# Kernel optimization log

Hardware: AMD Instinct MI355X
Metric: run time of the kernel (lower is better)

Reference implementation:

```python
import jax, jax.numpy as jnp
import numpy as np

B, T, C = 16, 2048, 68
HEAD = 64

def setup_inputs() -> dict:
    key = jax.random.key(0)
    k1, k2, k3, k4 = jax.random.split(key, 4)
    x = jax.random.normal(k1, (B, T, C), dtype=jnp.float32)
    # Linear(n_embd, head_size, bias=False): y = x @ W, W stored as [C, HEAD]
    Wk = jax.random.normal(k2, (C, HEAD), dtype=jnp.float32) / np.sqrt(C)
    Wq = jax.random.normal(k3, (C, HEAD), dtype=jnp.float32) / np.sqrt(C)
    Wv = jax.random.normal(k4, (C, HEAD), dtype=jnp.float32) / np.sqrt(C)
    return {"x": x, "Wk": Wk, "Wq": Wq, "Wv": Wv}

def reference(x, Wk, Wq, Wv):
    # single-head attention, no causal mask, dropout p=0.0 (identity)
    k = jnp.einsum('btc,ch->bth', x, Wk)   # [B,T,H]
    q = jnp.einsum('btc,ch->bth', x, Wq)   # [B,T,H]
    v = jnp.einsum('btc,ch->bth', x, Wv)   # [B,T,H]
    scale = 1.0 / jnp.sqrt(jnp.asarray(k.shape[-1], k.dtype))
    wei = jnp.einsum('bqh,bkh->bqk', q, k) * scale  # [B,T,T]
    wei = jax.nn.softmax(wei, axis=-1)
    out = jnp.einsum('bqk,bkh->bqh', wei, v)        # [B,T,H]
    return out
```

## Files before the change

### kernel.cpp

```cpp
#include <hip/hip_runtime.h>
#include <hip/hip_bf16.h>

#define BB 16
#define TT 2048
#define CC 68
#define HH 64

typedef short short8 __attribute__((ext_vector_type(8)));
typedef float floatx4 __attribute__((ext_vector_type(4)));

static __device__ __forceinline__ unsigned short f2bf(float f) {
    union { float f; unsigned u; } v; v.f = f;
    unsigned r = v.u + 0x7fffu + ((v.u >> 16) & 1u);
    return (unsigned short)(r >> 16);
}
static __device__ __forceinline__ unsigned pk2(float a, float b) {
    unsigned ua = __builtin_bit_cast(unsigned, a) + 0x8000u;
    unsigned ub = __builtin_bit_cast(unsigned, b) + 0x8000u;
    return (ua >> 16) | (ub & 0xffff0000u);
}
static __device__ __forceinline__ unsigned cvtpk(float a, float b) {
    unsigned r;
    asm("v_cvt_pk_bf16_f32 %0, %1, %2" : "=v"(r) : "v"(a), "v"(b));
    return r;
}

#define GLD16(gsrc, ldsbase)                                                        \
    __builtin_amdgcn_global_load_lds(                                               \
        (const __attribute__((address_space(1))) unsigned int*)(gsrc),              \
        (__attribute__((address_space(3))) unsigned int*)(ldsbase), 16, 0, 0)

#define WAITV4 asm volatile("s_waitcnt vmcnt(4)" ::: "memory")
#define WAITV0 asm volatile("s_waitcnt vmcnt(0)" ::: "memory")
#define BAR    asm volatile("s_barrier" ::: "memory")

__global__ __launch_bounds__(256) void prep_w(
        const float* __restrict__ Wk, const float* __restrict__ Wq,
        const float* __restrict__ Wv, unsigned short* __restrict__ Wt) {
    int idx = blockIdx.x * 256 + threadIdx.x;
    if (idx >= 192 * 96) return;
    int n = idx / 96, c = idx - n * 96;
    float v = 0.f;
    if (c < CC) {
        if (n < 64)       v = Wk[c * 64 + n];
        else if (n < 128) v = Wq[c * 64 + (n - 64)] * 0.18033688011112042f;
        else              v = Wv[c * 64 + (n - 128)];
    }
    Wt[idx] = f2bf(v);
}

__global__ __launch_bounds__(256) void qkv_kernel(
        const float* __restrict__ x, const unsigned short* __restrict__ Wt,
        unsigned short* __restrict__ Qb, unsigned short* __restrict__ Kb,
        unsigned short* __restrict__ Vt) {
    int tid = threadIdx.x;
    int wave = tid >> 6, lane = tid & 63, quad = lane >> 4, l15 = lane & 15;
    int id = blockIdx.x;
    int b = id & 15, rowblk = id >> 4;
    size_t row0 = (size_t)b * TT + rowblk * 64;
    int t0 = rowblk * 64;
    size_t myrow = row0 + wave * 16 + l15;
    const float* xr = x + myrow * CC;

    short8 a[3];
    union { short8 s8; unsigned u[4]; } t;
    #pragma unroll
    for (int cs = 0; cs < 2; ++cs) {
        float4 f0 = *(const float4*)(xr + cs * 32 + quad * 8);
        float4 f1 = *(const float4*)(xr + cs * 32 + quad * 8 + 4);
        t.u[0] = pk2(f0.x, f0.y); t.u[1] = pk2(f0.z, f0.w);
        t.u[2] = pk2(f1.x, f1.y); t.u[3] = pk2(f1.z, f1.w);
        a[cs] = t.s8;
    }
    {
        t.u[0] = 0; t.u[1] = 0; t.u[2] = 0; t.u[3] = 0;
        if (quad == 0) {
            float4 f = *(const float4*)(xr + 64);
            t.u[0] = pk2(f.x, f.y); t.u[1] = pk2(f.z, f.w);
        }
        a[2] = t.s8;
    }

    auto loadW = [&](short8 (&w)[3], int nt) {
        #pragma unroll
        for (int cs = 0; cs < 3; ++cs)
            w[cs] = *(const short8*)&Wt[(nt * 16 + l15) * 96 + cs * 32 + quad * 8];
    };

    short8 wf[3][3];
    loadW(wf[0], 0);
    loadW(wf[1], 1);
    #pragma unroll
    for (int nt = 0; nt < 12; ++nt) {
        if (nt + 2 < 12) loadW(wf[(nt + 2) % 3], nt + 2);
        floatx4 acc = (floatx4){0.f, 0.f, 0.f, 0.f};
        #pragma unroll
        for (int cs = 0; cs < 3; ++cs)
            acc = __builtin_amdgcn_mfma_f32_16x16x32_bf16(a[cs], wf[nt % 3][cs], acc, 0, 0, 0);

        if (nt < 8) {
            unsigned short* dst = (nt < 4) ? Kb : Qb;
            int h = (nt & 3) * 16 + l15;
            #pragma unroll
            for (int r = 0; r < 4; ++r)
                dst[(row0 + wave * 16 + quad * 4 + r) * 64 + h] = f2bf(acc[r]);
        } else {
            int h = (nt - 8) * 16 + l15;
            int tt = t0 + wave * 16 + quad * 4;
            uint2 v2; v2.x = pk2(acc[0], acc[1]); v2.y = pk2(acc[2], acc[3]);
            *(uint2*)&Vt[((size_t)(b * 64 + h)) * TT + tt] = v2;
        }
    }
}

__global__ __launch_bounds__(512, 2) void attn_kernel(
        const unsigned short* __restrict__ Qb,
        const unsigned short* __restrict__ Kb,
        const unsigned short* __restrict__ Vt,
        float* __restrict__ out) {
    __shared__ union {
        unsigned char stg[2][3][8192];
        float accL[128][66];
    } u;
    __shared__ float lL[2][128];

    int tid = threadIdx.x;
    int wave = tid >> 6, lane = tid & 63, quad = lane >> 4, l15 = lane & 15;
    int half = wave >> 2, qh = wave & 3;
    int id = blockIdx.x;
    int b = id & 15, qblk = id >> 4;
    int q0 = qblk * 128 + qh * 32;
    int kbase = half * 1024;

    short8 qf[2][2];
    #pragma unroll
    for (int qs = 0; qs < 2; ++qs)
        #pragma unroll
        for (int kh = 0; kh < 2; ++kh)
            qf[qs][kh] = *(const short8*)&Qb[((size_t)(b * TT + q0 + qs * 16 + l15)) * 64
                                             + kh * 32 + quad * 8];

    floatx4 acc[2][4];
    float lpart[2] = {0.f, 0.f};
    #pragma unroll
    for (int qs = 0; qs < 2; ++qs)
        #pragma unroll
        for (int hb = 0; hb < 4; ++hb) acc[qs][hb] = (floatx4){0.f, 0.f, 0.f, 0.f};

    auto stage = [&](int it, int p) {
        int kt = kbase + it * 32;
        if (qh == 0) {
            unsigned char* base = u.stg[half][p];
            #pragma unroll
            for (int i = 0; i < 4; ++i) {
                int ci = i * 64 + lane;
                int kv = ci >> 3, cp = ci & 7, c = cp ^ (kv & 7);
                GLD16(Kb + ((size_t)(b * TT + kt + kv) * 64 + c * 8), base + i * 1024);
            }
        } else if (qh == 1) {
            unsigned char* base = u.stg[half][p] + 4096;
            #pragma unroll
            for (int i = 0; i < 4; ++i) {
                int ci = i * 64 + lane;
                int h = ci >> 2, cp = ci & 3, c = cp ^ ((h >> 1) & 3);
                GLD16(Vt + ((size_t)(b * 64 + h) * TT + kt + c * 8), base + i * 1024);
            }
        }
    };

    auto compute = [&](int p) {
        const unsigned char* Kbuf = u.stg[half][p];
        const unsigned char* Vbuf = Kbuf + 4096;

        short8 kf[2][2], vf[4];
        #pragma unroll
        for (int ks = 0; ks < 2; ++ks)
            #pragma unroll
            for (int kh = 0; kh < 2; ++kh) {
                int cp = (kh * 4 + quad) ^ (l15 & 7);
                kf[ks][kh] = *(const short8*)(Kbuf + (ks * 16 + l15) * 128 + cp * 16);
            }
        #pragma unroll
        for (int hb = 0; hb < 4; ++hb) {
            int cp = quad ^ ((l15 >> 1) & 3);
            vf[hb] = *(const short8*)(Vbuf + (hb * 16 + l15) * 64 + cp * 16);
        }

        floatx4 s[2][2];
        #pragma unroll
        for (int qs = 0; qs < 2; ++qs)
            #pragma unroll
            for (int ks = 0; ks < 2; ++ks) {
                floatx4 z = (floatx4){0.f, 0.f, 0.f, 0.f};
                z = __builtin_amdgcn_mfma_f32_16x16x32_bf16(kf[ks][0], qf[qs][0], z, 0, 0, 0);
                z = __builtin_amdgcn_mfma_f32_16x16x32_bf16(kf[ks][1], qf[qs][1], z, 0, 0, 0);
                s[qs][ks] = z;
            }

        #pragma unroll
        for (int qs = 0; qs < 2; ++qs) {
            unsigned c00, c01, c10, c11;
            float lp = 0.f;
            {
                float e0 = __builtin_amdgcn_exp2f(s[qs][0][0]);
                float e1 = __builtin_amdgcn_exp2f(s[qs][0][1]);
                float e2 = __builtin_amdgcn_exp2f(s[qs][0][2]);
                float e3 = __builtin_amdgcn_exp2f(s[qs][0][3]);
                lp += (e0 + e1) + (e2 + e3);
                c00 = cvtpk(e0, e1); c01 = cvtpk(e2, e3);
            }
            {
                float e0 = __builtin_amdgcn_exp2f(s[qs][1][0]);
                float e1 = __builtin_amdgcn_exp2f(s[qs][1][1]);
                float e2 = __builtin_amdgcn_exp2f(s[qs][1][2]);
                float e3 = __builtin_amdgcn_exp2f(s[qs][1][3]);
                lp += (e0 + e1) + (e2 + e3);
                c10 = cvtpk(e0, e1); c11 = cvtpk(e2, e3);
            }
            lpart[qs] += lp;

            asm("v_permlane32_swap_b32 %0, %1" : "+v"(c00), "+v"(c10));
            asm("v_permlane16_swap_b32 %0, %1" : "+v"(c00), "+v"(c10));
            asm("v_permlane32_swap_b32 %0, %1" : "+v"(c01), "+v"(c11));
            asm("v_permlane16_swap_b32 %0, %1" : "+v"(c01), "+v"(c11));

            union { short8 s8; unsigned w[4]; } pu;
            pu.w[0] = c00; pu.w[1] = c01; pu.w[2] = c10; pu.w[3] = c11;
            #pragma unroll
            for (int hb = 0; hb < 4; ++hb)
                acc[qs][hb] = __builtin_amdgcn_mfma_f32_16x16x32_bf16(pu.s8, vf[hb], acc[qs][hb], 0, 0, 0);
        }
    };

    stage(0, 0);
    stage(1, 1);
    for (int it = 0; it < 32; ++it) {
        if (qh < 2) {
            if (it < 31) { WAITV4; } else { WAITV0; }
        }
        BAR;
        if (it + 2 < 32) stage(it + 2, (it + 2) % 3);
        compute(it % 3);
    }

    #pragma unroll
    for (int qs = 0; qs < 2; ++qs) {
        float v = lpart[qs];
        v += __shfl_xor(v, 16);
        v += __shfl_xor(v, 32);
        lpart[qs] = v;
    }
    if (quad == 0) {
        lL[half][qh * 32 + l15]      = lpart[0];
        lL[half][qh * 32 + 16 + l15] = lpart[1];
    }
    __syncthreads();

    if (half == 1) {
        #pragma unroll
        for (int qs = 0; qs < 2; ++qs)
            #pragma unroll
            for (int hb = 0; hb < 4; ++hb)
                #pragma unroll
                for (int r = 0; r < 4; ++r)
                    u.accL[qh * 32 + qs * 16 + quad * 4 + r][hb * 16 + l15] = acc[qs][hb][r];
    }
    __syncthreads();

    if (half == 0) {
        #pragma unroll
        for (int qs = 0; qs < 2; ++qs) {
            float rl[4];
            #pragma unroll
            for (int r = 0; r < 4; ++r) {
                int qw = qh * 32 + qs * 16 + quad * 4 + r;
                rl[r] = 1.0f / (lL[0][qw] + lL[1][qw]);
            }
            #pragma unroll
            for (int hb = 0; hb < 4; ++hb)
                #pragma unroll
                for (int r = 0; r < 4; ++r) {
                    int qw = qh * 32 + qs * 16 + quad * 4 + r;
                    float tot = acc[qs][hb][r] + u.accL[qw][hb * 16 + l15];
                    out[((size_t)(b * TT + qblk * 128 + qw)) * 64 + hb * 16 + l15] = tot * rl[r];
                }
        }
    }
}

extern "C" void kernel_launch(void* const* d_in, const int* in_sizes, int n_in,
                              void* d_out, int out_size, void* d_ws, size_t ws_size,
                              hipStream_t stream) {
    const float* x  = (const float*)d_in[0];
    const float* Wk = (const float*)d_in[1];
    const float* Wq = (const float*)d_in[2];
    const float* Wv = (const float*)d_in[3];

    unsigned short* Qb = (unsigned short*)d_ws;
    unsigned short* Kb = Qb + (size_t)BB * TT * HH;
    unsigned short* Vt = Kb + (size_t)BB * TT * HH;
    unsigned short* Wt = Vt + (size_t)BB * TT * HH;
    float* out = (float*)d_out;

    prep_w<<<dim3(72), dim3(256), 0, stream>>>(Wk, Wq, Wv, Wt);
    qkv_kernel<<<dim3(BB * TT / 64), dim3(256), 0, stream>>>(x, Wt, Qb, Kb, Vt);
    attn_kernel<<<dim3(BB * (TT / 128)), dim3(512), 0, stream>>>(Qb, Kb, Vt, out);
}
```

Measured before the change: 101.6 us.

## Halve attention query tile to 64 rows per block for more blocks

Each wave now handles 16 query rows instead of 32, so each attention block covers 64 queries and twice as many blocks are launched (512 instead of 256). Launch bounds are raised to allow 4 blocks per CU. The aim is better CU occupancy and latency hiding on a GPU with 256 CUs. The cost is that each K/V tile staged in shared memory is reused by half as many queries, which doubles global K/V traffic per query.

```diff
diff --git a/kernel.cpp b/kernel.cpp
--- a/kernel.cpp
+++ b/kernel.cpp
@@ -113,39 +113,34 @@
     }
 }
 
-__global__ __launch_bounds__(512, 2) void attn_kernel(
+__global__ __launch_bounds__(512, 4) void attn_kernel(
         const unsigned short* __restrict__ Qb,
         const unsigned short* __restrict__ Kb,
         const unsigned short* __restrict__ Vt,
         float* __restrict__ out) {
     __shared__ union {
         unsigned char stg[2][3][8192];
-        float accL[128][66];
+        float accL[64][66];
     } u;
-    __shared__ float lL[2][128];
+    __shared__ float lL[2][64];
 
     int tid = threadIdx.x;
     int wave = tid >> 6, lane = tid & 63, quad = lane >> 4, l15 = lane & 15;
     int half = wave >> 2, qh = wave & 3;
     int id = blockIdx.x;
     int b = id & 15, qblk = id >> 4;
-    int q0 = qblk * 128 + qh * 32;
+    int q0 = qblk * 64 + qh * 16;
     int kbase = half * 1024;
 
-    short8 qf[2][2];
-    #pragma unroll
-    for (int qs = 0; qs < 2; ++qs)
-        #pragma unroll
-        for (int kh = 0; kh < 2; ++kh)
-            qf[qs][kh] = *(const short8*)&Qb[((size_t)(b * TT + q0 + qs * 16 + l15)) * 64
-                                             + kh * 32 + quad * 8];
-
-    floatx4 acc[2][4];
-    float lpart[2] = {0.f, 0.f};
-    #pragma unroll
-    for (int qs = 0; qs < 2; ++qs)
-        #pragma unroll
-        for (int hb = 0; hb < 4; ++hb) acc[qs][hb] = (floatx4){0.f, 0.f, 0.f, 0.f};
+    short8 qf[2];
+    #pragma unroll
+    for (int kh = 0; kh < 2; ++kh)
+        qf[kh] = *(const short8*)&Qb[((size_t)(b * TT + q0 + l15)) * 64 + kh * 32 + quad * 8];
+
+    floatx4 acc[4];
+    float lpart = 0.f;
+    #pragma unroll
+    for (int hb = 0; hb < 4; ++hb) acc[hb] = (floatx4){0.f, 0.f, 0.f, 0.f};
 
     auto stage = [&](int it, int p) {
         int kt = kbase + it * 32;
@@ -186,50 +181,43 @@
             vf[hb] = *(const short8*)(Vbuf + (hb * 16 + l15) * 64 + cp * 16);
         }
 
-        floatx4 s[2][2];
-        #pragma unroll
-        for (int qs = 0; qs < 2; ++qs)
-            #pragma unroll
-            for (int ks = 0; ks < 2; ++ks) {
-                floatx4 z = (floatx4){0.f, 0.f, 0.f, 0.f};
-                z = __builtin_amdgcn_mfma_f32_16x16x32_bf16(kf[ks][0], qf[qs][0], z, 0, 0, 0);
-                z = __builtin_amdgcn_mfma_f32_16x16x32_bf16(kf[ks][1], qf[qs][1], z, 0, 0, 0);
-                s[qs][ks] = z;
-            }
-
-        #pragma unroll
-        for (int qs = 0; qs < 2; ++qs) {
-            unsigned c00, c01, c10, c11;
-            float lp = 0.f;
-            {
-                float e0 = __builtin_amdgcn_exp2f(s[qs][0][0]);
-                float e1 = __builtin_amdgcn_exp2f(s[qs][0][1]);
-                float e2 = __builtin_amdgcn_exp2f(s[qs][0][2]);
-                float e3 = __builtin_amdgcn_exp2f(s[qs][0][3]);
-                lp += (e0 + e1) + (e2 + e3);
-                c00 = cvtpk(e0, e1); c01 = cvtpk(e2, e3);
-            }
-            {
-                float e0 = __builtin_amdgcn_exp2f(s[qs][1][0]);
-                float e1 = __builtin_amdgcn_exp2f(s[qs][1][1]);
-                float e2 = __builtin_amdgcn_exp2f(s[qs][1][2]);
-                float e3 = __builtin_amdgcn_exp2f(s[qs][1][3]);
-                lp += (e0 + e1) + (e2 + e3);
-                c10 = cvtpk(e0, e1); c11 = cvtpk(e2, e3);
-            }
-            lpart[qs] += lp;
-
-            asm("v_permlane32_swap_b32 %0, %1" : "+v"(c00), "+v"(c10));
-            asm("v_permlane16_swap_b32 %0, %1" : "+v"(c00), "+v"(c10));
-            asm("v_permlane32_swap_b32 %0, %1" : "+v"(c01), "+v"(c11));
-            asm("v_permlane16_swap_b32 %0, %1" : "+v"(c01), "+v"(c11));
-
-            union { short8 s8; unsigned w[4]; } pu;
-            pu.w[0] = c00; pu.w[1] = c01; pu.w[2] = c10; pu.w[3] = c11;
-            #pragma unroll
-            for (int hb = 0; hb < 4; ++hb)
-                acc[qs][hb] = __builtin_amdgcn_mfma_f32_16x16x32_bf16(pu.s8, vf[hb], acc[qs][hb], 0, 0, 0);
-        }
+        floatx4 s[2];
+        #pragma unroll
+        for (int ks = 0; ks < 2; ++ks) {
+            floatx4 z = (floatx4){0.f, 0.f, 0.f, 0.f};
+            z = __builtin_amdgcn_mfma_f32_16x16x32_bf16(kf[ks][0], qf[0], z, 0, 0, 0);
+            z = __builtin_amdgcn_mfma_f32_16x16x32_bf16(kf[ks][1], qf[1], z, 0, 0, 0);
+            s[ks] = z;
+        }
+
+        unsigned c00, c01, c10, c11;
+        {
+            float e0 = __builtin_amdgcn_exp2f(s[0][0]);
+            float e1 = __builtin_amdgcn_exp2f(s[0][1]);
+            float e2 = __builtin_amdgcn_exp2f(s[0][2]);
+            float e3 = __builtin_amdgcn_exp2f(s[0][3]);
+            lpart += (e0 + e1) + (e2 + e3);
+            c00 = cvtpk(e0, e1); c01 = cvtpk(e2, e3);
+        }
+        {
+            float e0 = __builtin_amdgcn_exp2f(s[1][0]);
+            float e1 = __builtin_amdgcn_exp2f(s[1][1]);
+            float e2 = __builtin_amdgcn_exp2f(s[1][2]);
+            float e3 = __builtin_amdgcn_exp2f(s[1][3]);
+            lpart += (e0 + e1) + (e2 + e3);
+            c10 = cvtpk(e0, e1); c11 = cvtpk(e2, e3);
+        }
+
+        asm("v_permlane32_swap_b32 %0, %1" : "+v"(c00), "+v"(c10));
+        asm("v_permlane16_swap_b32 %0, %1" : "+v"(c00), "+v"(c10));
+        asm("v_permlane32_swap_b32 %0, %1" : "+v"(c01), "+v"(c11));
+        asm("v_permlane16_swap_b32 %0, %1" : "+v"(c01), "+v"(c11));
+
+        union { short8 s8; unsigned w[4]; } pu;
+        pu.w[0] = c00; pu.w[1] = c01; pu.w[2] = c10; pu.w[3] = c11;
+        #pragma unroll
+        for (int hb = 0; hb < 4; ++hb)
+            acc[hb] = __builtin_amdgcn_mfma_f32_16x16x32_bf16(pu.s8, vf[hb], acc[hb], 0, 0, 0);
     };
 
     stage(0, 0);
@@ -243,48 +231,38 @@
         compute(it % 3);
     }
 
-    #pragma unroll
-    for (int qs = 0; qs < 2; ++qs) {
-        float v = lpart[qs];
+    {
+        float v = lpart;
         v += __shfl_xor(v, 16);
         v += __shfl_xor(v, 32);
-        lpart[qs] = v;
-    }
-    if (quad == 0) {
-        lL[half][qh * 32 + l15]      = lpart[0];
-        lL[half][qh * 32 + 16 + l15] = lpart[1];
+        if (quad == 0) lL[half][qh * 16 + l15] = v;
     }
     __syncthreads();
 
     if (half == 1) {
         #pragma unroll
-        for (int qs = 0; qs < 2; ++qs)
-            #pragma unroll
-            for (int hb = 0; hb < 4; ++hb)
-                #pragma unroll
-                for (int r = 0; r < 4; ++r)
-                    u.accL[qh * 32 + qs * 16 + quad * 4 + r][hb * 16 + l15] = acc[qs][hb][r];
+        for (int hb = 0; hb < 4; ++hb)
+            #pragma unroll
+            for (int r = 0; r < 4; ++r)
+                u.accL[qh * 16 + quad * 4 + r][hb * 16 + l15] = acc[hb][r];
     }
     __syncthreads();
 
     if (half == 0) {
-        #pragma unroll
-        for (int qs = 0; qs < 2; ++qs) {
-            float rl[4];
+        float rl[4];
+        #pragma unroll
+        for (int r = 0; r < 4; ++r) {
+            int qw = qh * 16 + quad * 4 + r;
+            rl[r] = 1.0f / (lL[0][qw] + lL[1][qw]);
+        }
+        #pragma unroll
+        for (int hb = 0; hb < 4; ++hb)
             #pragma unroll
             for (int r = 0; r < 4; ++r) {
-                int qw = qh * 32 + qs * 16 + quad * 4 + r;
-                rl[r] = 1.0f / (lL[0][qw] + lL[1][qw]);
-            }
-            #pragma unroll
-            for (int hb = 0; hb < 4; ++hb)
-                #pragma unroll
-                for (int r = 0; r < 4; ++r) {
-                    int qw = qh * 32 + qs * 16 + quad * 4 + r;
-                    float tot = acc[qs][hb][r] + u.accL[qw][hb * 16 + l15];
-                    out[((size_t)(b * TT + qblk * 128 + qw)) * 64 + hb * 16 + l15] = tot * rl[r];
-                }
-        }
+                int qw = qh * 16 + quad * 4 + r;
+                float tot = acc[hb][r] + u.accL[qw][hb * 16 + l15];
+                out[((size_t)(b * TT + qblk * 64 + qw)) * 64 + hb * 16 + l15] = tot * rl[r];
+            }
     }
 }
 
@@ -304,5 +282,5 @@
 
     prep_w<<<dim3(72), dim3(256), 0, stream>>>(Wk, Wq, Wv, Wt);
     qkv_kernel<<<dim3(BB * TT / 64), dim3(256), 0, stream>>>(x, Wt, Qb, Kb, Vt);
-    attn_kernel<<<dim3(BB * (TT / 128)), dim3(512), 0, stream>>>(Qb, Kb, Vt, out);
-}
+    attn_kernel<<<dim3(BB * (TT / 64)), dim3(512), 0, stream>>>(Qb, Kb, Vt, out);
+}
```

Result: no change. 100.8 us (-0.8%).
